# Optimization experiments

Measured on AMD Instinct MI355X. Metric: run time of the kernel, lower is better.

## Reference

```python
import jax, jax.numpy as jnp
import numpy as np


def setup_inputs() -> dict:
    key = jax.random.key(0)
    k1, k2, k3 = jax.random.split(key, 3)
    N, C, S = 8192, 256, 7
    D = C * S * S            # 12544 flattened RoI feature dim
    NUM_CLASSES = 81         # includes background (softmax cls head)
    x = jax.random.normal(k1, (N, C, S, S), dtype=jnp.float32)
    # fc weights ~ N(0, 0.01) like mmdet's normal init
    W_cls = jax.random.normal(k2, (NUM_CLASSES, D), dtype=jnp.float32) * 0.01
    b_cls = jnp.zeros((NUM_CLASSES,), dtype=jnp.float32)
    W_reg = jax.random.normal(k3, (4 * NUM_CLASSES, D), dtype=jnp.float32) * 0.001
    b_reg = jnp.zeros((4 * NUM_CLASSES,), dtype=jnp.float32)
    return {"x": x, "W_cls": W_cls, "b_cls": b_cls, "W_reg": W_reg, "b_reg": b_reg}


def reference(x, W_cls, b_cls, W_reg, b_reg):
    # BBoxHead.forward: flatten RoI features, then cls / reg FC heads.
    N = x.shape[0]
    feat = x.reshape(N, -1)                      # [N, C*S*S]
    cls_score = feat @ W_cls.T + b_cls           # [N, num_classes]
    bbox_pred = feat @ W_reg.T + b_reg           # [N, 4*num_classes]
    return cls_score, bbox_pred
```

## Files before the change

### kernel.cpp

```cpp
#include <hip/hip_runtime.h>
#include <stdint.h>
#include <stddef.h>

#define K_FULL 12544
#define M_ROWS 8192
#define NCLS 81
#define NREG 324
#define NTOT 405
#define NPAD 416
#define OUT0 663552
#define OUT_TOTAL 3317760

typedef __bf16 bf16x8 __attribute__((ext_vector_type(8)));
typedef float floatx4 __attribute__((ext_vector_type(4)));

__device__ __forceinline__ uint32_t pack2_bf16(float a, float b) {
  uint32_t ua = __float_as_uint(a);
  uint32_t ub = __float_as_uint(b);
  ua = (ua + 0x7FFFu + ((ua >> 16) & 1u)) >> 16;
  ub = (ub + 0x7FFFu + ((ub >> 16) & 1u)) >> 16;
  return ua | (ub << 16);
}

__global__ void pack_w(const float* __restrict__ Wc, const float* __restrict__ Wr,
                       uint16_t* __restrict__ Wb) {
  const int u = blockIdx.x * blockDim.x + threadIdx.x;
  if (u >= (K_FULL / 8)) return;
  const int row = blockIdx.y;
  uint4 v = {0u, 0u, 0u, 0u};
  const float* src = nullptr;
  if (row < NCLS) src = Wc + (size_t)row * K_FULL;
  else if (row < NTOT) src = Wr + (size_t)(row - NCLS) * K_FULL;
  if (src) {
    const float4 f0 = *(const float4*)(src + u * 8);
    const float4 f1 = *(const float4*)(src + u * 8 + 4);
    v.x = pack2_bf16(f0.x, f0.y);
    v.y = pack2_bf16(f0.z, f0.w);
    v.z = pack2_bf16(f1.x, f1.y);
    v.w = pack2_bf16(f1.z, f1.w);
  }
  *(uint4*)(Wb + (size_t)row * K_FULL + u * 8) = v;
}

__global__ void bias_init(const float* __restrict__ bc, const float* __restrict__ br,
                          float* __restrict__ out) {
  const int i = blockIdx.x * blockDim.x + threadIdx.x;
  if (i >= OUT_TOTAL) return;
  if (i < OUT0) {
    out[i] = bc[i % NCLS];
  } else {
    const int j = i - OUT0;
    out[i] = br[j % NREG];
  }
}

__global__ __launch_bounds__(512, 4) void gemm_kernel(
    const float* __restrict__ x, const uint16_t* __restrict__ Wb,
    float* __restrict__ out) {
  __shared__ uint4 sA4[512];
  __shared__ uint4 sB4[3328];
  uint8_t* sA = (uint8_t*)sA4;
  uint8_t* sB = (uint8_t*)sB4;

  const int tid = threadIdx.x;
  const int lane = tid & 63;
  const int wave = tid >> 6;
  const int mg = wave >> 1;
  const int ng = wave & 1;

  const int mt = blockIdx.x >> 2;
  const int ks = blockIdx.x & 3;
  const int rowBase = mt * 64;
  int k0 = ks * 3136;
  const int kEnd = k0 + 3136;

  floatx4 acc[13];
  const floatx4 zero = {0.0f, 0.0f, 0.0f, 0.0f};
#pragma unroll
  for (int j = 0; j < 13; ++j) acc[j] = zero;

  const int mA = tid >> 3;
  const int pA = tid & 7;
  const int kbA = pA ^ (mA & 7);
  const float* gA = x + (size_t)(rowBase + mA) * K_FULL + k0 + kbA * 8;

  const int rB = lane >> 3;
  const int pB = lane & 7;
  const int kbB = pB ^ rB;

  float4 pf0 = *(const float4*)gA;
  float4 pf1 = *(const float4*)(gA + 4);
  gA += 64;

  for (; k0 < kEnd; k0 += 64) {
    __syncthreads();

    {
      uint4 v;
      v.x = pack2_bf16(pf0.x, pf0.y);
      v.y = pack2_bf16(pf0.z, pf0.w);
      v.z = pack2_bf16(pf1.x, pf1.y);
      v.w = pack2_bf16(pf1.z, pf1.w);
      *(uint4*)(sA + mA * 128 + pA * 16) = v;
    }

    for (int i = wave; i < 52; i += 8) {
      const int n = i * 8 + rB;
      const uint16_t* g = Wb + (size_t)n * K_FULL + (k0 + kbB * 8);
      __builtin_amdgcn_global_load_lds(
          (const __attribute__((address_space(1))) void*)g,
          (__attribute__((address_space(3))) void*)(sB + i * 1024), 16, 0, 0);
    }

    __syncthreads();

    if (k0 + 64 < kEnd) {
      pf0 = *(const float4*)gA;
      pf1 = *(const float4*)(gA + 4);
      gA += 64;
    }

    const int q = lane >> 4;
    const int m0 = mg * 16 + (lane & 15);
#pragma unroll
    for (int s = 0; s < 2; ++s) {
      const int kb = s * 4 + q;
      const bf16x8 a0 = *(const bf16x8*)(sA + m0 * 128 + ((kb ^ (m0 & 7)) * 16));
#pragma unroll
      for (int nf = 0; nf < 13; ++nf) {
        const int n = ng * 208 + nf * 16 + (lane & 15);
        const bf16x8 b = *(const bf16x8*)(sB + n * 128 + ((kb ^ (n & 7)) * 16));
        acc[nf] = __builtin_amdgcn_mfma_f32_16x16x32_bf16(a0, b, acc[nf], 0, 0, 0);
      }
    }
  }

  const int q = lane >> 4;
  const int c0 = lane & 15;
  const int r0 = rowBase + mg * 16 + q * 4;
#pragma unroll
  for (int nf = 0; nf < 13; ++nf) {
    const int col = ng * 208 + nf * 16 + c0;
    if (col < NCLS) {
      float* dst = out + (size_t)r0 * NCLS + col;
#pragma unroll
      for (int r = 0; r < 4; ++r)
        unsafeAtomicAdd(dst + (size_t)r * NCLS, acc[nf][r]);
    } else if (col < NTOT) {
      float* dst = out + OUT0 + (size_t)r0 * NREG + (col - NCLS);
#pragma unroll
      for (int r = 0; r < 4; ++r)
        unsafeAtomicAdd(dst + (size_t)r * NREG, acc[nf][r]);
    }
  }
}

extern "C" void kernel_launch(void* const* d_in, const int* in_sizes, int n_in,
                              void* d_out, int out_size, void* d_ws, size_t ws_size,
                              hipStream_t stream) {
  const float* x = (const float*)d_in[0];
  const float* Wc = (const float*)d_in[1];
  const float* bc = (const float*)d_in[2];
  const float* Wr = (const float*)d_in[3];
  const float* br = (const float*)d_in[4];
  float* out = (float*)d_out;
  uint16_t* Wb = (uint16_t*)d_ws;

  pack_w<<<dim3(7, 416), dim3(256), 0, stream>>>(Wc, Wr, Wb);
  bias_init<<<dim3((OUT_TOTAL + 255) / 256), dim3(256), 0, stream>>>(bc, br, out);
  gemm_kernel<<<dim3(512), dim3(512), 0, stream>>>(x, Wb, out);
}
```

Measured before the change: 657.8 us.

## Double-buffer weight tiles in LDS and load A straight into registers

The GEMM now uses a 32-wide K chunk with a double-buffered LDS tile for the bf16 weights. Each chunk's weight loads are issued before the current chunk's MFMAs run. The A operand (x rows) is no longer staged through LDS: each wave loads its own fp32 rows, converts them to bf16 in registers, and prefetches the next chunk. The wave layout changes to 2x4, with two M fragments by seven N fragments per wave, so each B fragment is reused across two A fragments. Each loop iteration now does half as much K work, and the weight padding grows to 448 rows.

```diff
diff --git a/kernel.cpp b/kernel.cpp
--- a/kernel.cpp
+++ b/kernel.cpp
@@ -7,9 +7,11 @@
 #define NCLS 81
 #define NREG 324
 #define NTOT 405
-#define NPAD 416
+#define NPAD 448
 #define OUT0 663552
 #define OUT_TOTAL 3317760
+#define KSPLIT 3136
+#define NCHUNK 98
 
 typedef __bf16 bf16x8 __attribute__((ext_vector_type(8)));
 typedef float floatx4 __attribute__((ext_vector_type(4)));
@@ -46,111 +48,110 @@
                           float* __restrict__ out) {
   const int i = blockIdx.x * blockDim.x + threadIdx.x;
   if (i >= OUT_TOTAL) return;
-  if (i < OUT0) {
-    out[i] = bc[i % NCLS];
-  } else {
-    const int j = i - OUT0;
-    out[i] = br[j % NREG];
-  }
+  if (i < OUT0) out[i] = bc[i % NCLS];
+  else out[i] = br[(i - OUT0) % NREG];
 }
 
 __global__ __launch_bounds__(512, 4) void gemm_kernel(
     const float* __restrict__ x, const uint16_t* __restrict__ Wb,
     float* __restrict__ out) {
-  __shared__ uint4 sA4[512];
-  __shared__ uint4 sB4[3328];
-  uint8_t* sA = (uint8_t*)sA4;
-  uint8_t* sB = (uint8_t*)sB4;
+  __shared__ uint8_t sB[2][28672];
 
   const int tid = threadIdx.x;
   const int lane = tid & 63;
   const int wave = tid >> 6;
-  const int mg = wave >> 1;
-  const int ng = wave & 1;
+  const int mg = wave >> 2;
+  const int ng = wave & 3;
 
   const int mt = blockIdx.x >> 2;
   const int ks = blockIdx.x & 3;
   const int rowBase = mt * 64;
-  int k0 = ks * 3136;
-  const int kEnd = k0 + 3136;
+  const int k0 = ks * KSPLIT;
 
-  floatx4 acc[13];
+  const int i15 = lane & 15;
+  const int q = lane >> 4;
+
+  floatx4 acc[2][7];
   const floatx4 zero = {0.0f, 0.0f, 0.0f, 0.0f};
 #pragma unroll
-  for (int j = 0; j < 13; ++j) acc[j] = zero;
+  for (int i = 0; i < 2; ++i)
+#pragma unroll
+    for (int j = 0; j < 7; ++j) acc[i][j] = zero;
 
-  const int mA = tid >> 3;
-  const int pA = tid & 7;
-  const int kbA = pA ^ (mA & 7);
-  const float* gA = x + (size_t)(rowBase + mA) * K_FULL + k0 + kbA * 8;
+  const float* gA0 = x + (size_t)(rowBase + mg * 32 + i15) * K_FULL + k0 + q * 8;
+  const float* gA1 = gA0 + (size_t)16 * K_FULL;
 
-  const int rB = lane >> 3;
-  const int pB = lane & 7;
-  const int kbB = pB ^ rB;
+  const uint16_t* gB = Wb + (size_t)(lane >> 2) * K_FULL + k0 + (lane & 3) * 8;
 
-  float4 pf0 = *(const float4*)gA;
-  float4 pf1 = *(const float4*)(gA + 4);
-  gA += 64;
+#pragma unroll
+  for (int u = 0; u < 4; ++u) {
+    const int uu = wave + u * 8;
+    if (uu < 28)
+      __builtin_amdgcn_global_load_lds(
+          (const __attribute__((address_space(1))) void*)(gB + (size_t)uu * 16 * K_FULL),
+          (__attribute__((address_space(3))) void*)(&sB[0][uu * 1024]), 16, 0, 0);
+  }
+  float4 pf0 = *(const float4*)gA0;
+  float4 pf1 = *(const float4*)(gA0 + 4);
+  float4 pf2 = *(const float4*)gA1;
+  float4 pf3 = *(const float4*)(gA1 + 4);
 
-  for (; k0 < kEnd; k0 += 64) {
-    __syncthreads();
-
-    {
-      uint4 v;
-      v.x = pack2_bf16(pf0.x, pf0.y);
-      v.y = pack2_bf16(pf0.z, pf0.w);
-      v.z = pack2_bf16(pf1.x, pf1.y);
-      v.w = pack2_bf16(pf1.z, pf1.w);
-      *(uint4*)(sA + mA * 128 + pA * 16) = v;
-    }
-
-    for (int i = wave; i < 52; i += 8) {
-      const int n = i * 8 + rB;
-      const uint16_t* g = Wb + (size_t)n * K_FULL + (k0 + kbB * 8);
-      __builtin_amdgcn_global_load_lds(
-          (const __attribute__((address_space(1))) void*)g,
-          (__attribute__((address_space(3))) void*)(sB + i * 1024), 16, 0, 0);
-    }
+  for (int c = 0; c < NCHUNK; ++c) {
+    const int cur = c & 1;
+    const int cn = (c + 1 < NCHUNK) ? (c + 1) : (NCHUNK - 1);
 
     __syncthreads();
 
-    if (k0 + 64 < kEnd) {
-      pf0 = *(const float4*)gA;
-      pf1 = *(const float4*)(gA + 4);
-      gA += 64;
+#pragma unroll
+    for (int u = 0; u < 4; ++u) {
+      const int uu = wave + u * 8;
+      if (uu < 28)
+        __builtin_amdgcn_global_load_lds(
+            (const __attribute__((address_space(1))) void*)(gB + (size_t)uu * 16 * K_FULL + cn * 32),
+            (__attribute__((address_space(3))) void*)(&sB[cur ^ 1][uu * 1024]), 16, 0, 0);
     }
 
-    const int q = lane >> 4;
-    const int m0 = mg * 16 + (lane & 15);
+    bf16x8 a0, a1;
+    a0[0] = (__bf16)pf0.x; a0[1] = (__bf16)pf0.y; a0[2] = (__bf16)pf0.z; a0[3] = (__bf16)pf0.w;
+    a0[4] = (__bf16)pf1.x; a0[5] = (__bf16)pf1.y; a0[6] = (__bf16)pf1.z; a0[7] = (__bf16)pf1.w;
+    a1[0] = (__bf16)pf2.x; a1[1] = (__bf16)pf2.y; a1[2] = (__bf16)pf2.z; a1[3] = (__bf16)pf2.w;
+    a1[4] = (__bf16)pf3.x; a1[5] = (__bf16)pf3.y; a1[6] = (__bf16)pf3.z; a1[7] = (__bf16)pf3.w;
+
+    {
+      const float* nA0 = gA0 + cn * 32;
+      const float* nA1 = gA1 + cn * 32;
+      pf0 = *(const float4*)nA0;
+      pf1 = *(const float4*)(nA0 + 4);
+      pf2 = *(const float4*)nA1;
+      pf3 = *(const float4*)(nA1 + 4);
+    }
+
+    const uint8_t* bbase = &sB[cur][0] + (ng * 112 + i15) * 64 + q * 16;
 #pragma unroll
-    for (int s = 0; s < 2; ++s) {
-      const int kb = s * 4 + q;
-      const bf16x8 a0 = *(const bf16x8*)(sA + m0 * 128 + ((kb ^ (m0 & 7)) * 16));
-#pragma unroll
-      for (int nf = 0; nf < 13; ++nf) {
-        const int n = ng * 208 + nf * 16 + (lane & 15);
-        const bf16x8 b = *(const bf16x8*)(sB + n * 128 + ((kb ^ (n & 7)) * 16));
-        acc[nf] = __builtin_amdgcn_mfma_f32_16x16x32_bf16(a0, b, acc[nf], 0, 0, 0);
-      }
+    for (int f = 0; f < 7; ++f) {
+      const bf16x8 b = *(const bf16x8*)(bbase + f * 1024);
+      acc[0][f] = __builtin_amdgcn_mfma_f32_16x16x32_bf16(a0, b, acc[0][f], 0, 0, 0);
+      acc[1][f] = __builtin_amdgcn_mfma_f32_16x16x32_bf16(a1, b, acc[1][f], 0, 0, 0);
     }
   }
 
-  const int q = lane >> 4;
-  const int c0 = lane & 15;
-  const int r0 = rowBase + mg * 16 + q * 4;
 #pragma unroll
-  for (int nf = 0; nf < 13; ++nf) {
-    const int col = ng * 208 + nf * 16 + c0;
-    if (col < NCLS) {
-      float* dst = out + (size_t)r0 * NCLS + col;
+  for (int fm = 0; fm < 2; ++fm) {
+    const int r0 = rowBase + mg * 32 + fm * 16 + q * 4;
 #pragma unroll
-      for (int r = 0; r < 4; ++r)
-        unsafeAtomicAdd(dst + (size_t)r * NCLS, acc[nf][r]);
-    } else if (col < NTOT) {
-      float* dst = out + OUT0 + (size_t)r0 * NREG + (col - NCLS);
+    for (int f = 0; f < 7; ++f) {
+      const int col = ng * 112 + f * 16 + i15;
+      if (col < NCLS) {
+        float* dst = out + (size_t)r0 * NCLS + col;
 #pragma unroll
-      for (int r = 0; r < 4; ++r)
-        unsafeAtomicAdd(dst + (size_t)r * NREG, acc[nf][r]);
+        for (int r = 0; r < 4; ++r)
+          unsafeAtomicAdd(dst + (size_t)r * NCLS, acc[fm][f][r]);
+      } else if (col < NTOT) {
+        float* dst = out + OUT0 + (size_t)r0 * NREG + (col - NCLS);
+#pragma unroll
+        for (int r = 0; r < 4; ++r)
+          unsafeAtomicAdd(dst + (size_t)r * NREG, acc[fm][f][r]);
+      }
     }
   }
 }
@@ -166,7 +167,7 @@
   float* out = (float*)d_out;
   uint16_t* Wb = (uint16_t*)d_ws;
 
-  pack_w<<<dim3(7, 416), dim3(256), 0, stream>>>(Wc, Wr, Wb);
+  pack_w<<<dim3(7, NPAD), dim3(256), 0, stream>>>(Wc, Wr, Wb);
   bias_init<<<dim3((OUT_TOTAL + 255) / 256), dim3(256), 0, stream>>>(bc, br, out);
   gemm_kernel<<<dim3(512), dim3(512), 0, stream>>>(x, Wb, out);
 }
```

New measurement: 814.3 us. +23.8%, slower.
